# Kernel tuning notes

Hardware: AMD Instinct MI355X
Metric: run time of the kernel (lower is better)

Reference implementation:

```python
import jax, jax.numpy as jnp
import numpy as np

N, NFEAT, NHID, NCLASS, NHEADS = 4096, 512, 64, 40, 8
ALPHA = 0.2  # LeakyReLU negative slope
NEG_BIG = -9e15


def _xavier(key, shape, gain=1.414):
    fan_in, fan_out = shape[0], shape[1]
    bound = gain * np.sqrt(6.0 / (fan_in + fan_out))
    return jax.random.uniform(key, shape, jnp.float32, -bound, bound)


def setup_inputs() -> dict:
    key = jax.random.key(0)
    ks = jax.random.split(key, 6)
    x = jax.random.normal(ks[0], (N, NFEAT), jnp.float32)
    adj = jax.random.randint(ks[1], (N, N), 0, 2).astype(jnp.float32)
    # per-head params of the 8 input GAT layers
    Ws = _xavier(ks[2], (NHEADS, NFEAT, NHID))          # stacked W: [H, F, D]
    a_s = _xavier(ks[3], (NHEADS, 2 * NHID, 1))[..., 0]  # [H, 2D]
    # output GAT layer (concat=False)
    W_out = _xavier(ks[4], (NHID * NHEADS, NCLASS))
    a_out = _xavier(ks[5], (2 * NCLASS, 1))[..., 0]      # [2C]
    return {"x": x, "adj": adj, "Ws": Ws, "a_s": a_s, "W_out": W_out, "a_out": a_out}


def _gat_layer(inp, adj_mask, W, a, concat):
    # h = inp @ W : [N, D]
    h = inp @ W
    D = h.shape[1]
    a1, a2 = a[:D], a[D:]
    # e[i,j] = leakyrelu(a . [h_i, h_j]) = leakyrelu(h_i.a1 + h_j.a2)
    # (same math as the N*N*2D concat in the original, without materializing it)
    f1 = h @ a1  # [N]
    f2 = h @ a2  # [N]
    e = jax.nn.leaky_relu(f1[:, None] + f2[None, :], negative_slope=ALPHA)
    att = jax.nn.softmax(jnp.where(adj_mask, e, NEG_BIG), axis=1)
    h_prime = att @ h  # [N, D]
    return jax.nn.elu(h_prime) if concat else h_prime


def reference(x, adj, Ws, a_s, W_out, a_out):
    adj_mask = adj > 0
    # 8 attention heads over the input features (eval mode: dropout is identity)
    heads = jax.vmap(lambda W, a: _gat_layer(x, adj_mask, W, a, True))(Ws, a_s)  # [H, N, D]
    x2 = jnp.transpose(heads, (1, 0, 2)).reshape(N, NHEADS * NHID)  # concat along feature dim
    out = _gat_layer(x2, adj_mask, W_out, a_out, False)  # [N, C]
    out = jax.nn.elu(out)
    return jax.nn.log_softmax(out, axis=1)
```

## Files before the change

kernel.cpp:

```cpp
#include <hip/hip_runtime.h>
#include <hip/hip_bf16.h>
#include <stdint.h>

#define NN 4096
#define NF 512
#define NH 64
#define NCLS 40
#define NHEADS 8
#define LOG2E 1.4426950408889634f

typedef __attribute__((ext_vector_type(8))) short bh8;
typedef __attribute__((ext_vector_type(4))) float f32x4;

__device__ __forceinline__ unsigned short f2bu(float f) {
    union { float f; unsigned u; } v; v.f = f;
    unsigned r = (v.u + 0x7FFFu + ((v.u >> 16) & 1u)) >> 16;
    return (unsigned short)r;
}
__device__ __forceinline__ float lrelu(float x) { return fmaxf(x, 0.2f * x); }
__device__ __forceinline__ float elu1(float x) { return x > 0.f ? x : expm1f(x); }
__device__ __forceinline__ float exp2fast(float x) {
    float r; asm("v_exp_f32 %0, %1" : "=v"(r) : "v"(x)); return r;
}
__device__ __forceinline__ unsigned fenc(float f) {
    unsigned u = __builtin_bit_cast(unsigned, f);
    return ((int)u < 0) ? ~u : (u | 0x80000000u);
}
__device__ __forceinline__ float fdec(unsigned k) {
    unsigned u = (k & 0x80000000u) ? (k ^ 0x80000000u) : ~k;
    return __builtin_bit_cast(float, u);
}
__device__ __forceinline__ int sbfe1(unsigned v, int off) {
#if __has_builtin(__builtin_amdgcn_sbfe)
    return __builtin_amdgcn_sbfe((int)v, off, 1);
#else
    return ((int)(v << (31 - off))) >> 31;
#endif
}
__device__ __forceinline__ float bmask(float p, unsigned mdw, int bit) {
    return __builtin_bit_cast(float,
        __builtin_bit_cast(unsigned, p) & (unsigned)sbfe1(mdw, bit));
}

__global__ void prep_all_k(const float* __restrict__ x, const float* __restrict__ Ws,
                           const float* __restrict__ Wo,
                           unsigned short* __restrict__ xb, unsigned short* __restrict__ WT,
                           unsigned short* __restrict__ WoT) {
    int idx = blockIdx.x * 256 + threadIdx.x;
    if (idx < 2097152) {
        xb[idx] = f2bu(x[idx]);
    } else if (idx < 2097152 + 262144) {
        int j = idx - 2097152;
        int c = j >> 9, k = j & 511;
        WT[j] = f2bu(Ws[(size_t)(c >> 6) * (NF * NH) + (size_t)k * NH + (c & 63)]);
    } else if (idx < 2097152 + 262144 + 24576) {
        int j = idx - 2359296;
        int c = j >> 9, k = j & 511;
        WoT[j] = f2bu(c < NCLS ? Wo[(size_t)k * NCLS + c] : 0.f);
    }
}
__global__ __launch_bounds__(256) void prep_adj_k(const float* __restrict__ adj,
                                                  unsigned char* __restrict__ adjp,
                                                  unsigned* __restrict__ FM1u,
                                                  unsigned* __restrict__ FM2u) {
    if (blockIdx.x == 0) {
        if (threadIdx.x < 8) FM1u[threadIdx.x] = 0u;
        if (threadIdx.x == 8) FM2u[0] = 0u;
    }
    int w = threadIdx.x >> 6, lane = threadIdx.x & 63;
    int i = blockIdx.x * 4 + w;
    const float* row = adj + (size_t)i * NN;
    for (int t = 0; t < 64; ++t) {
        uint64_t m = __ballot(row[t * 64 + lane] > 0.f);
        if (lane < 8) {
            unsigned char mb = (unsigned char)(m >> (8 * lane));
            int grp = lane & 3, jt = 2 * t + (lane >> 2);
            adjp[((size_t)i * 4 + grp) * 128 + jt] = mb;
        }
    }
}

__device__ __forceinline__ unsigned pack2(float x, float y) {
    unsigned ux = __builtin_bit_cast(unsigned, x), uy = __builtin_bit_cast(unsigned, y);
    ux += 0x7FFFu + ((ux >> 16) & 1u);
    uy += 0x7FFFu + ((uy >> 16) & 1u);
    return __builtin_amdgcn_perm(uy, ux, 0x07060302u);
}

__global__ __launch_bounds__(256) void gemm1_k(const unsigned short* __restrict__ xb,
                                               const unsigned short* __restrict__ WT,
                                               const float* __restrict__ a_s,
                                               unsigned short* __restrict__ Bp1,
                                               float* __restrict__ f1L,
                                               float* __restrict__ f2L,
                                               unsigned* __restrict__ FM1u) {
    __shared__ unsigned short xs[64 * 40];
    __shared__ unsigned short wsm[64 * 40];
    const int tid = threadIdx.x;
    const int w = tid >> 6, lane = tid & 63, r16 = lane & 15, grp = lane >> 4;
    const int i0 = blockIdx.x << 6, h = blockIdx.y, c0 = h << 6;
    const int srow = tid >> 2, sseg = tid & 3;
    const unsigned short* xsrc = xb + (size_t)(i0 + srow) * NF + sseg * 8;
    const unsigned short* wsrc = WT + (size_t)(c0 + srow) * NF + sseg * 8;
    f32x4 a0 = {0,0,0,0}, a1 = {0,0,0,0}, a2 = {0,0,0,0}, a3 = {0,0,0,0};
    bh8 rx = *(const bh8*)(xsrc), rw = *(const bh8*)(wsrc);
    for (int kb = 0; kb < NF; kb += 32) {
        *(bh8*)(xs + srow * 40 + sseg * 8) = rx;
        *(bh8*)(wsm + srow * 40 + sseg * 8) = rw;
        __syncthreads();
        if (kb + 32 < NF) { rx = *(const bh8*)(xsrc + kb + 32); rw = *(const bh8*)(wsrc + kb + 32); }
        bh8 af = *(const bh8*)(xs + (w * 16 + r16) * 40 + grp * 8);
        bh8 b0 = *(const bh8*)(wsm + (r16) * 40 + grp * 8);
        bh8 b1 = *(const bh8*)(wsm + (16 + r16) * 40 + grp * 8);
        bh8 b2 = *(const bh8*)(wsm + (32 + r16) * 40 + grp * 8);
        bh8 b3 = *(const bh8*)(wsm + (48 + r16) * 40 + grp * 8);
        a0 = __builtin_amdgcn_mfma_f32_16x16x32_bf16(af, b0, a0, 0, 0, 0);
        a1 = __builtin_amdgcn_mfma_f32_16x16x32_bf16(af, b1, a1, 0, 0, 0);
        a2 = __builtin_amdgcn_mfma_f32_16x16x32_bf16(af, b2, a2, 0, 0, 0);
        a3 = __builtin_amdgcn_mfma_f32_16x16x32_bf16(af, b3, a3, 0, 0, 0);
        __syncthreads();
    }
    const int jt = (i0 >> 5) + (w >> 1);
    const int kg = ((w & 1) << 1) + (grp >> 1);
    const int lanep = kg * 16 + r16;
    const int ebase = (grp & 1) * 4;
    unsigned short* bp = Bp1 + ((size_t)(h * 128 + jt)) * 2048 + lanep * 8 + ebase;
    {
        uint2 v;
        v.x = pack2(a0[0], a0[1]); v.y = pack2(a0[2], a0[3]); *(uint2*)(bp + 0 * 512) = v;
        v.x = pack2(a1[0], a1[1]); v.y = pack2(a1[2], a1[3]); *(uint2*)(bp + 1 * 512) = v;
        v.x = pack2(a2[0], a2[1]); v.y = pack2(a2[2], a2[3]); *(uint2*)(bp + 2 * 512) = v;
        v.x = pack2(a3[0], a3[1]); v.y = pack2(a3[2], a3[3]); *(uint2*)(bp + 3 * 512) = v;
    }
    const float* ap = a_s + h * 128;
    float a1v[4], a2v[4];
#pragma unroll
    for (int n = 0; n < 4; ++n) { a1v[n] = ap[r16 + 16 * n]; a2v[n] = ap[64 + r16 + 16 * n]; }
    float wmax = -3.0e38f;
#pragma unroll
    for (int r = 0; r < 4; ++r) {
        const int orow = i0 + w * 16 + grp * 4 + r;
        float s1 = a0[r] * a1v[0] + a1[r] * a1v[1] + a2[r] * a1v[2] + a3[r] * a1v[3];
        float s2 = a0[r] * a2v[0] + a1[r] * a2v[1] + a2[r] * a2v[2] + a3[r] * a2v[3];
#pragma unroll
        for (int o2 = 1; o2 < 16; o2 <<= 1) { s1 += __shfl_xor(s1, o2); s2 += __shfl_xor(s2, o2); }
        s1 *= LOG2E; s2 *= LOG2E;
        if (r16 == 0) { f1L[h * NN + orow] = s1; f2L[h * NN + orow] = s2; }
        wmax = fmaxf(wmax, s2);
    }
    wmax = fmaxf(wmax, __shfl_xor(wmax, 16));
    wmax = fmaxf(wmax, __shfl_xor(wmax, 32));
    if (lane == 0) atomicMax(&FM1u[h], fenc(wmax));
}

__global__ __launch_bounds__(256) void gemm2_k(const unsigned short* __restrict__ x2b,
                                               const unsigned short* __restrict__ WoT,
                                               const float* __restrict__ a_out,
                                               unsigned short* __restrict__ Bp2,
                                               float* __restrict__ f12L,
                                               float* __restrict__ f22L,
                                               unsigned* __restrict__ FM2u) {
    __shared__ unsigned short xs[64 * 40];
    __shared__ unsigned short wsm[48 * 40];
    const int tid = threadIdx.x;
    const int w = tid >> 6, lane = tid & 63, r16 = lane & 15, grp = lane >> 4;
    const int i0 = blockIdx.x << 6;
    const int srow = tid >> 2, sseg = tid & 3;
    const unsigned short* xsrc = x2b + (size_t)(i0 + srow) * NF + sseg * 8;
    const unsigned short* wsrc = WoT + (size_t)srow * NF + sseg * 8;
    f32x4 a0 = {0,0,0,0}, a1 = {0,0,0,0}, a2 = {0,0,0,0};
    bh8 rx = *(const bh8*)(xsrc);
    bh8 rw; if (tid < 192) rw = *(const bh8*)(wsrc);
    for (int kb = 0; kb < NF; kb += 32) {
        *(bh8*)(xs + srow * 40 + sseg * 8) = rx;
        if (tid < 192) *(bh8*)(wsm + srow * 40 + sseg * 8) = rw;
        __syncthreads();
        if (kb + 32 < NF) {
            rx = *(const bh8*)(xsrc + kb + 32);
            if (tid < 192) rw = *(const bh8*)(wsrc + kb + 32);
        }
        bh8 af = *(const bh8*)(xs + (w * 16 + r16) * 40 + grp * 8);
        bh8 b0 = *(const bh8*)(wsm + (r16) * 40 + grp * 8);
        bh8 b1 = *(const bh8*)(wsm + (16 + r16) * 40 + grp * 8);
        bh8 b2 = *(const bh8*)(wsm + (32 + r16) * 40 + grp * 8);
        a0 = __builtin_amdgcn_mfma_f32_16x16x32_bf16(af, b0, a0, 0, 0, 0);
        a1 = __builtin_amdgcn_mfma_f32_16x16x32_bf16(af, b1, a1, 0, 0, 0);
        a2 = __builtin_amdgcn_mfma_f32_16x16x32_bf16(af, b2, a2, 0, 0, 0);
        __syncthreads();
    }
    const int jt = (i0 >> 5) + (w >> 1);
    const int kg = ((w & 1) << 1) + (grp >> 1);
    const int lanep = kg * 16 + r16;
    const int ebase = (grp & 1) * 4;
    unsigned short* bp = Bp2 + (size_t)jt * 1536 + lanep * 8 + ebase;
    {
        uint2 v;
        v.x = pack2(a0[0], a0[1]); v.y = pack2(a0[2], a0[3]); *(uint2*)(bp + 0 * 512) = v;
        v.x = pack2(a1[0], a1[1]); v.y = pack2(a1[2], a1[3]); *(uint2*)(bp + 1 * 512) = v;
        v.x = pack2(a2[0], a2[1]); v.y = pack2(a2[2], a2[3]); *(uint2*)(bp + 2 * 512) = v;
    }
    float a1v[3], a2v[3];
#pragma unroll
    for (int n = 0; n < 3; ++n) {
        int col = r16 + 16 * n;
        a1v[n] = col < NCLS ? a_out[col] : 0.f;
        a2v[n] = col < NCLS ? a_out[NCLS + col] : 0.f;
    }
    float wmax = -3.0e38f;
#pragma unroll
    for (int r = 0; r < 4; ++r) {
        const int orow = i0 + w * 16 + grp * 4 + r;
        float s1 = a0[r] * a1v[0] + a1[r] * a1v[1] + a2[r] * a1v[2];
        float s2 = a0[r] * a2v[0] + a1[r] * a2v[1] + a2[r] * a2v[2];
#pragma unroll
        for (int o2 = 1; o2 < 16; o2 <<= 1) { s1 += __shfl_xor(s1, o2); s2 += __shfl_xor(s2, o2); }
        s1 *= LOG2E; s2 *= LOG2E;
        if (r16 == 0) { f12L[orow] = s1; f22L[orow] = s2; }
        wmax = fmaxf(wmax, s2);
    }
    wmax = fmaxf(wmax, __shfl_xor(wmax, 16));
    wmax = fmaxf(wmax, __shfl_xor(wmax, 32));
    if (lane == 0) atomicMax(&FM2u[0], fenc(wmax));
}

__global__ __launch_bounds__(512, 4) void attn1_k(const unsigned short* __restrict__ Bp1,
                                                  const unsigned char* __restrict__ adjp,
                                                  const float* __restrict__ f1L,
                                                  const float* __restrict__ f2L,
                                                  const unsigned* __restrict__ FM1u,
                                                  unsigned short* __restrict__ x2b) {
    __shared__ float EFs[8192];
    __shared__ unsigned ADJd[64 * 4 * 33];
    const int tid = threadIdx.x, w = tid >> 6, lane = tid & 63;
    const int r16 = lane & 15, grp = lane >> 4;
    const int rowg = w & 3, jq = w >> 2;
    const int h = blockIdx.y;
    const int i0 = blockIdx.x * 64;
    const float fm = fdec(FM1u[h]);
    const float* f2p = f2L + h * NN;
    for (int t = 0; t < 8; ++t) {
        int j = tid + t * 512;
        float d = f2p[j] - fm;
        EFs[2 * j] = exp2fast(d);
        EFs[2 * j + 1] = exp2fast(0.2f * d);
    }
    {
        const unsigned* asrc = (const unsigned*)(adjp + (size_t)i0 * 512);
        for (int t = 0; t < 16; ++t) {
            int idx = tid + t * 512;
            ADJd[(idx >> 5) * 33 + (idx & 31)] = asrc[idx];
        }
    }
    const int irow = i0 + rowg * 16 + r16;
    const float f1v = f1L[h * NN + irow];
    const float mL = lrelu(f1v + fm);
    const float A = exp2fast(f1v + fm - mL);
    const float B = exp2fast(__builtin_fmaf(0.2f, f1v + fm, -mL));
    __syncthreads();
    const unsigned* adjrd = ADJd + ((rowg * 16 + r16) * 4 + grp) * 33 + jq * 16;
    const float* efp = EFs + grp * 16;
    const unsigned short* Bbase = Bp1 + (size_t)h * 128 * 2048 + lane * 8;
    f32x4 acc0 = {0,0,0,0}, acc1 = {0,0,0,0}, acc2 = {0,0,0,0}, acc3 = {0,0,0,0}, accd = {0,0,0,0};
    const short ov = (r16 == 0) ? (short)0x3F80 : (short)0;
    bh8 ones;
#pragma unroll
    for (int e = 0; e < 8; ++e) ones[e] = ov;
    bh8 nb0, nb1, nb2, nb3;
#define PREF1(JT) { const unsigned short* Bn = Bbase + (size_t)(JT) * 2048;              \
        nb0 = *(const bh8*)(Bn);        nb1 = *(const bh8*)(Bn + 512);                    \
        nb2 = *(const bh8*)(Bn + 1024); nb3 = *(const bh8*)(Bn + 1536); }
    const int jtbase = jq * 64;
    PREF1(jtbase);
    for (int jt4 = 0; jt4 < 16; ++jt4) {
        const unsigned mdw = adjrd[jt4];
#pragma unroll
        for (int u = 0; u < 4; ++u) {
            const int jt = jtbase + jt4 * 4 + u;
            bh8 b0 = nb0, b1 = nb1, b2 = nb2, b3 = nb3;
            PREF1(jt + 1);
            const float* e4 = efp + jt * 64;
            float4 ea = *(const float4*)(e4);
            float4 eb = *(const float4*)(e4 + 4);
            float4 ec = *(const float4*)(e4 + 8);
            float4 ed = *(const float4*)(e4 + 12);
            const int bb = u * 8;
            union { bh8 v; unsigned u32[4]; } pk;
            {
                float p0 = bmask(fmaxf(A * ea.x, B * ea.y), mdw, bb + 0);
                float p1 = bmask(fmaxf(A * ea.z, B * ea.w), mdw, bb + 1);
                pk.u32[0] = __builtin_amdgcn_perm(__builtin_bit_cast(unsigned, p1),
                                                  __builtin_bit_cast(unsigned, p0), 0x07060302u);
                float p2 = bmask(fmaxf(A * eb.x, B * eb.y), mdw, bb + 2);
                float p3 = bmask(fmaxf(A * eb.z, B * eb.w), mdw, bb + 3);
                pk.u32[1] = __builtin_amdgcn_perm(__builtin_bit_cast(unsigned, p3),
                                                  __builtin_bit_cast(unsigned, p2), 0x07060302u);
                float p4 = bmask(fmaxf(A * ec.x, B * ec.y), mdw, bb + 4);
                float p5 = bmask(fmaxf(A * ec.z, B * ec.w), mdw, bb + 5);
                pk.u32[2] = __builtin_amdgcn_perm(__builtin_bit_cast(unsigned, p5),
                                                  __builtin_bit_cast(unsigned, p4), 0x07060302u);
                float p6 = bmask(fmaxf(A * ed.x, B * ed.y), mdw, bb + 6);
                float p7 = bmask(fmaxf(A * ed.z, B * ed.w), mdw, bb + 7);
                pk.u32[3] = __builtin_amdgcn_perm(__builtin_bit_cast(unsigned, p7),
                                                  __builtin_bit_cast(unsigned, p6), 0x07060302u);
            }
            acc0 = __builtin_amdgcn_mfma_f32_16x16x32_bf16(pk.v, b0, acc0, 0, 0, 0);
            acc1 = __builtin_amdgcn_mfma_f32_16x16x32_bf16(pk.v, b1, acc1, 0, 0, 0);
            acc2 = __builtin_amdgcn_mfma_f32_16x16x32_bf16(pk.v, b2, acc2, 0, 0, 0);
            acc3 = __builtin_amdgcn_mfma_f32_16x16x32_bf16(pk.v, b3, acc3, 0, 0, 0);
            accd = __builtin_amdgcn_mfma_f32_16x16x32_bf16(pk.v, ones, accd, 0, 0, 0);
        }
    }
#undef PREF1
    __syncthreads();
    float (*comb)[64][20] = (float(*)[64][20])EFs;
    if (jq == 1) {
        float* cb = &comb[rowg][lane][0];
#pragma unroll
        for (int r = 0; r < 4; ++r) {
            cb[r] = acc0[r]; cb[4 + r] = acc1[r]; cb[8 + r] = acc2[r];
            cb[12 + r] = acc3[r]; cb[16 + r] = accd[r];
        }
    }
    __syncthreads();
    if (jq == 0) {
        const float* cb = &comb[rowg][lane][0];
#pragma unroll
        for (int r = 0; r < 4; ++r) {
            acc0[r] += cb[r]; acc1[r] += cb[4 + r]; acc2[r] += cb[8 + r];
            acc3[r] += cb[12 + r]; accd[r] += cb[16 + r];
        }
#pragma unroll
        for (int r = 0; r < 4; ++r) {
            const float den = __shfl(accd[r], lane & 48);
            const float inv = 1.0f / den;
            unsigned short* o = x2b + (size_t)(i0 + rowg * 16 + grp * 4 + r) * NF + h * 64 + r16;
            o[0]  = f2bu(elu1(acc0[r] * inv));
            o[16] = f2bu(elu1(acc1[r] * inv));
            o[32] = f2bu(elu1(acc2[r] * inv));
            o[48] = f2bu(elu1(acc3[r] * inv));
        }
    }
}

__global__ __launch_bounds__(256, 4) void attn2_k(const unsigned short* __restrict__ Bp2,
                                                  const unsigned char* __restrict__ adjp,
                                                  const float* __restrict__ f12L,
                                                  const float* __restrict__ f22L,
                                                  const unsigned* __restrict__ FM2u,
                                                  float* __restrict__ Pa2) {
    __shared__ float EFs[1024];
    const int tid = threadIdx.x, w = tid >> 6, lane = tid & 63;
    const int r16 = lane & 15, grp = lane >> 4;
    const int ch = blockIdx.y;
    const int i0 = blockIdx.x * 64 + w * 16;
    const int i = i0 + r16;
    const float fm = fdec(FM2u[0]);
    for (int t = 0; t < 2; ++t) {
        int j = tid + t * 256;
        float d = f22L[ch * 512 + j] - fm;
        EFs[2 * j] = exp2fast(d);
        EFs[2 * j + 1] = exp2fast(0.2f * d);
    }
    const float f1v = f12L[i];
    const float mL = lrelu(f1v + fm);
    const float A = exp2fast(f1v + fm - mL);
    const float B = exp2fast(__builtin_fmaf(0.2f, f1v + fm, -mL));
    __syncthreads();
    const unsigned char* adjr = adjp + ((size_t)i * 4 + grp) * 128 + ch * 16;
    f32x4 acc0 = {0,0,0,0}, acc1 = {0,0,0,0}, acc2 = {0,0,0,0}, accd = {0,0,0,0};
    const short ov = (r16 == 0) ? (short)0x3F80 : (short)0;
    bh8 ones;
#pragma unroll
    for (int e = 0; e < 8; ++e) ones[e] = ov;
    const int jt0 = ch * 16;
    const unsigned short* Bbase = Bp2 + lane * 8;
    const float* efp = EFs + grp * 16;
    bh8 nb0, nb1, nb2;
#define PREF2(JT) { const unsigned short* Bn = Bbase + (size_t)(JT) * 1536;              \
        nb0 = *(const bh8*)(Bn); nb1 = *(const bh8*)(Bn + 512); nb2 = *(const bh8*)(Bn + 1024); }
    PREF2(jt0);
    for (int jt4 = 0; jt4 < 4; ++jt4) {
        const unsigned mdw = *(const unsigned*)(adjr + jt4 * 4);
#pragma unroll
        for (int u = 0; u < 4; ++u) {
            const int ltj = jt4 * 4 + u;
            bh8 b0 = nb0, b1 = nb1, b2 = nb2;
            PREF2(jt0 + ltj + 1);
            const float* e4 = efp + ltj * 64;
            float4 ea = *(const float4*)(e4);
            float4 eb = *(const float4*)(e4 + 4);
            float4 ec = *(const float4*)(e4 + 8);
            float4 ed = *(const float4*)(e4 + 12);
            const int bb = u * 8;
            union { bh8 v; unsigned u32[4]; } pk;
            {
                float p0 = bmask(fmaxf(A * ea.x, B * ea.y), mdw, bb + 0);
                float p1 = bmask(fmaxf(A * ea.z, B * ea.w), mdw, bb + 1);
                pk.u32[0] = __builtin_amdgcn_perm(__builtin_bit_cast(unsigned, p1),
                                                  __builtin_bit_cast(unsigned, p0), 0x07060302u);
                float p2 = bmask(fmaxf(A * eb.x, B * eb.y), mdw, bb + 2);
                float p3 = bmask(fmaxf(A * eb.z, B * eb.w), mdw, bb + 3);
                pk.u32[1] = __builtin_amdgcn_perm(__builtin_bit_cast(unsigned, p3),
                                                  __builtin_bit_cast(unsigned, p2), 0x07060302u);
                float p4 = bmask(fmaxf(A * ec.x, B * ec.y), mdw, bb + 4);
                float p5 = bmask(fmaxf(A * ec.z, B * ec.w), mdw, bb + 5);
                pk.u32[2] = __builtin_amdgcn_perm(__builtin_bit_cast(unsigned, p5),
                                                  __builtin_bit_cast(unsigned, p4), 0x07060302u);
                float p6 = bmask(fmaxf(A * ed.x, B * ed.y), mdw, bb + 6);
                float p7 = bmask(fmaxf(A * ed.z, B * ed.w), mdw, bb + 7);
                pk.u32[3] = __builtin_amdgcn_perm(__builtin_bit_cast(unsigned, p7),
                                                  __builtin_bit_cast(unsigned, p6), 0x07060302u);
            }
            acc0 = __builtin_amdgcn_mfma_f32_16x16x32_bf16(pk.v, b0, acc0, 0, 0, 0);
            acc1 = __builtin_amdgcn_mfma_f32_16x16x32_bf16(pk.v, b1, acc1, 0, 0, 0);
            acc2 = __builtin_amdgcn_mfma_f32_16x16x32_bf16(pk.v, b2, acc2, 0, 0, 0);
            accd = __builtin_amdgcn_mfma_f32_16x16x32_bf16(pk.v, ones, accd, 0, 0, 0);
        }
    }
#undef PREF2
#pragma unroll
    for (int r = 0; r < 4; ++r) {
        const int row = i0 + grp * 4 + r;
        float* prow = Pa2 + ((size_t)ch * NN + row) * 52;
        prow[r16] = acc0[r];
        prow[16 + r16] = acc1[r];
        prow[32 + r16] = acc2[r];
        if (r16 == 0) prow[48] = accd[r];
    }
}

__global__ __launch_bounds__(256) void attn2fin_k(const float* __restrict__ Pa2,
                                                  float* __restrict__ out) {
    const int tid = threadIdx.x;
    const int row = blockIdx.x * 4 + (tid >> 6);
    const int lane = tid & 63;
    float s = 0.f;
    if (lane < 49) {
#pragma unroll
        for (int c = 0; c < 8; ++c) s += Pa2[((size_t)c * NN + row) * 52 + lane];
    }
    const float den = __shfl(s, 48);
    const float inv = 1.0f / den;
    float v = (lane < NCLS) ? elu1(s * inv) : -3.0e38f;
    float mx = v;
#pragma unroll
    for (int o = 1; o < 64; o <<= 1) mx = fmaxf(mx, __shfl_xor(mx, o));
    float ex = (lane < NCLS) ? __expf(v - mx) : 0.f;
#pragma unroll
    for (int o = 1; o < 64; o <<= 1) ex += __shfl_xor(ex, o);
    const float lse = mx + logf(ex);
    if (lane < NCLS) out[(size_t)row * NCLS + lane] = v - lse;
}

#define OFF_XB   0ULL
#define OFF_WT   4194304ULL
#define OFF_WOT  4718592ULL
#define OFF_BP1  4767744ULL
#define OFF_X2B  8962048ULL
#define OFF_BP2  13156352ULL
#define OFF_F1L  13549568ULL
#define OFF_F2L  13680640ULL
#define OFF_F12  13811712ULL
#define OFF_F22  13828096ULL
#define OFF_FM1  13844480ULL
#define OFF_FM2  13844736ULL
#define OFF_ADJ  13844992ULL
#define OFF_PA2  15942144ULL

extern "C" void kernel_launch(void* const* d_in, const int* in_sizes, int n_in,
                              void* d_out, int out_size, void* d_ws, size_t ws_size,
                              hipStream_t stream) {
    const float* x     = (const float*)d_in[0];
    const float* adj   = (const float*)d_in[1];
    const float* Ws    = (const float*)d_in[2];
    const float* a_s   = (const float*)d_in[3];
    const float* W_out = (const float*)d_in[4];
    const float* a_out = (const float*)d_in[5];
    float* out = (float*)d_out;
    char* w = (char*)d_ws;

    unsigned short* xb  = (unsigned short*)(w + OFF_XB);
    unsigned short* WT  = (unsigned short*)(w + OFF_WT);
    unsigned short* WoT = (unsigned short*)(w + OFF_WOT);
    unsigned short* Bp1 = (unsigned short*)(w + OFF_BP1);
    unsigned short* x2b = (unsigned short*)(w + OFF_X2B);
    unsigned short* Bp2 = (unsigned short*)(w + OFF_BP2);
    float* f1L = (float*)(w + OFF_F1L);
    float* f2L = (float*)(w + OFF_F2L);
    float* f12 = (float*)(w + OFF_F12);
    float* f22 = (float*)(w + OFF_F22);
    unsigned* FM1u = (unsigned*)(w + OFF_FM1);
    unsigned* FM2u = (unsigned*)(w + OFF_FM2);
    unsigned char* adjp = (unsigned char*)(w + OFF_ADJ);
    float* Pa2 = (float*)(w + OFF_PA2);

    prep_all_k<<<9312, 256, 0, stream>>>(x, Ws, W_out, xb, WT, WoT);
    prep_adj_k<<<1024, 256, 0, stream>>>(adj, adjp, FM1u, FM2u);

    gemm1_k<<<dim3(64, 8), 256, 0, stream>>>(xb, WT, a_s, Bp1, f1L, f2L, FM1u);
    attn1_k<<<dim3(64, 8), 512, 0, stream>>>(Bp1, adjp, f1L, f2L, FM1u, x2b);

    gemm2_k<<<64, 256, 0, stream>>>(x2b, WoT, a_out, Bp2, f12, f22, FM2u);
    attn2_k<<<dim3(64, 8), 256, 0, stream>>>(Bp2, adjp, f12, f22, FM2u, Pa2);
    attn2fin_k<<<1024, 256, 0, stream>>>(Pa2, out);
}
```

Before: 233.3 us.

## Merge prep kernels, fuse attn2 with finalize, drop LDS adjacency staging

Merges the adjacency bit-packing and the bf16 conversion kernels into one launch and vectorizes the adjacency reads and x conversion. gemm1 now uses 128-row tiles with 512 threads. attn1 reads adjacency masks straight from global memory instead of staging them in LDS, and its occupancy hint is raised. attn2 now does the column-chunk reduction in LDS inside the block and applies the log-softmax there, which removes the partial-sum buffer and the separate finalize kernel. This trades fewer launches and less global traffic for in-block tree reductions and fewer, larger attn2 blocks.

Measured after the change: 207.3 us. 11.2% less time.

```diff
diff --git a/kernel.cpp b/kernel.cpp
--- a/kernel.cpp
+++ b/kernel.cpp
@@ -41,45 +41,6 @@
     return __builtin_bit_cast(float,
         __builtin_bit_cast(unsigned, p) & (unsigned)sbfe1(mdw, bit));
 }
-
-__global__ void prep_all_k(const float* __restrict__ x, const float* __restrict__ Ws,
-                           const float* __restrict__ Wo,
-                           unsigned short* __restrict__ xb, unsigned short* __restrict__ WT,
-                           unsigned short* __restrict__ WoT) {
-    int idx = blockIdx.x * 256 + threadIdx.x;
-    if (idx < 2097152) {
-        xb[idx] = f2bu(x[idx]);
-    } else if (idx < 2097152 + 262144) {
-        int j = idx - 2097152;
-        int c = j >> 9, k = j & 511;
-        WT[j] = f2bu(Ws[(size_t)(c >> 6) * (NF * NH) + (size_t)k * NH + (c & 63)]);
-    } else if (idx < 2097152 + 262144 + 24576) {
-        int j = idx - 2359296;
-        int c = j >> 9, k = j & 511;
-        WoT[j] = f2bu(c < NCLS ? Wo[(size_t)k * NCLS + c] : 0.f);
-    }
-}
-__global__ __launch_bounds__(256) void prep_adj_k(const float* __restrict__ adj,
-                                                  unsigned char* __restrict__ adjp,
-                                                  unsigned* __restrict__ FM1u,
-                                                  unsigned* __restrict__ FM2u) {
-    if (blockIdx.x == 0) {
-        if (threadIdx.x < 8) FM1u[threadIdx.x] = 0u;
-        if (threadIdx.x == 8) FM2u[0] = 0u;
-    }
-    int w = threadIdx.x >> 6, lane = threadIdx.x & 63;
-    int i = blockIdx.x * 4 + w;
-    const float* row = adj + (size_t)i * NN;
-    for (int t = 0; t < 64; ++t) {
-        uint64_t m = __ballot(row[t * 64 + lane] > 0.f);
-        if (lane < 8) {
-            unsigned char mb = (unsigned char)(m >> (8 * lane));
-            int grp = lane & 3, jt = 2 * t + (lane >> 2);
-            adjp[((size_t)i * 4 + grp) * 128 + jt] = mb;
-        }
-    }
-}
-
 __device__ __forceinline__ unsigned pack2(float x, float y) {
     unsigned ux = __builtin_bit_cast(unsigned, x), uy = __builtin_bit_cast(unsigned, y);
     ux += 0x7FFFu + ((ux >> 16) & 1u);
@@ -87,28 +48,80 @@
     return __builtin_amdgcn_perm(uy, ux, 0x07060302u);
 }
 
-__global__ __launch_bounds__(256) void gemm1_k(const unsigned short* __restrict__ xb,
+__global__ __launch_bounds__(256) void prep_all_k(const float* __restrict__ x,
+                                                  const float* __restrict__ adj,
+                                                  const float* __restrict__ Ws,
+                                                  const float* __restrict__ Wo,
+                                                  unsigned short* __restrict__ xb,
+                                                  unsigned short* __restrict__ WT,
+                                                  unsigned short* __restrict__ WoT,
+                                                  unsigned char* __restrict__ adjp,
+                                                  unsigned* __restrict__ FM1u,
+                                                  unsigned* __restrict__ FM2u) {
+    const int bid = blockIdx.x, tid = threadIdx.x;
+    if (bid < 8192) {
+        __shared__ unsigned char sm[4][64];
+        const int i = bid >> 1, half = bid & 1;
+        const float* rp = adj + (size_t)i * NN + half * 2048 + tid * 8;
+        float4 v0 = ((const float4*)rp)[0];
+        float4 v1 = ((const float4*)rp)[1];
+        unsigned b = (v0.x > 0.f ? 1u : 0u) | (v0.y > 0.f ? 2u : 0u) |
+                     (v0.z > 0.f ? 4u : 0u) | (v0.w > 0.f ? 8u : 0u) |
+                     (v1.x > 0.f ? 16u : 0u) | (v1.y > 0.f ? 32u : 0u) |
+                     (v1.z > 0.f ? 64u : 0u) | (v1.w > 0.f ? 128u : 0u);
+        sm[tid & 3][tid >> 2] = (unsigned char)b;
+        __syncthreads();
+        if (tid < 64) {
+            int gp = tid >> 4, word = tid & 15;
+            unsigned d = *(const unsigned*)&sm[gp][word * 4];
+            *(unsigned*)(adjp + ((size_t)i * 4 + gp) * 128 + half * 64 + word * 4) = d;
+        }
+    } else if (bid < 10240) {
+        if (bid == 8192) {
+            if (tid < 8) FM1u[tid] = 0u;
+            if (tid == 8) FM2u[0] = 0u;
+        }
+        int t = (bid - 8192) * 256 + tid;
+        float4 v = ((const float4*)x)[t];
+        uint2 o; o.x = pack2(v.x, v.y); o.y = pack2(v.z, v.w);
+        ((uint2*)xb)[t] = o;
+    } else if (bid < 11264) {
+        int j = (bid - 10240) * 256 + tid;
+        int c = j >> 9, k = j & 511;
+        WT[j] = f2bu(Ws[(size_t)(c >> 6) * (NF * NH) + (size_t)k * NH + (c & 63)]);
+    } else {
+        int j = (bid - 11264) * 256 + tid;
+        int c = j >> 9, k = j & 511;
+        WoT[j] = f2bu(c < NCLS ? Wo[(size_t)k * NCLS + c] : 0.f);
+    }
+}
+
+__global__ __launch_bounds__(512) void gemm1_k(const unsigned short* __restrict__ xb,
                                                const unsigned short* __restrict__ WT,
                                                const float* __restrict__ a_s,
                                                unsigned short* __restrict__ Bp1,
                                                float* __restrict__ f1L,
                                                float* __restrict__ f2L,
                                                unsigned* __restrict__ FM1u) {
-    __shared__ unsigned short xs[64 * 40];
+    __shared__ unsigned short xs[128 * 40];
     __shared__ unsigned short wsm[64 * 40];
     const int tid = threadIdx.x;
     const int w = tid >> 6, lane = tid & 63, r16 = lane & 15, grp = lane >> 4;
-    const int i0 = blockIdx.x << 6, h = blockIdx.y, c0 = h << 6;
+    const int i0 = blockIdx.x << 7, h = blockIdx.y, c0 = h << 6;
     const int srow = tid >> 2, sseg = tid & 3;
     const unsigned short* xsrc = xb + (size_t)(i0 + srow) * NF + sseg * 8;
-    const unsigned short* wsrc = WT + (size_t)(c0 + srow) * NF + sseg * 8;
+    const unsigned short* wsrc = WT + (size_t)(c0 + (srow & 63)) * NF + sseg * 8;
     f32x4 a0 = {0,0,0,0}, a1 = {0,0,0,0}, a2 = {0,0,0,0}, a3 = {0,0,0,0};
-    bh8 rx = *(const bh8*)(xsrc), rw = *(const bh8*)(wsrc);
+    bh8 rx = *(const bh8*)(xsrc);
+    bh8 rw; if (tid < 256) rw = *(const bh8*)(wsrc);
     for (int kb = 0; kb < NF; kb += 32) {
         *(bh8*)(xs + srow * 40 + sseg * 8) = rx;
-        *(bh8*)(wsm + srow * 40 + sseg * 8) = rw;
+        if (tid < 256) *(bh8*)(wsm + srow * 40 + sseg * 8) = rw;
         __syncthreads();
-        if (kb + 32 < NF) { rx = *(const bh8*)(xsrc + kb + 32); rw = *(const bh8*)(wsrc + kb + 32); }
+        if (kb + 32 < NF) {
+            rx = *(const bh8*)(xsrc + kb + 32);
+            if (tid < 256) rw = *(const bh8*)(wsrc + kb + 32);
+        }
         bh8 af = *(const bh8*)(xs + (w * 16 + r16) * 40 + grp * 8);
         bh8 b0 = *(const bh8*)(wsm + (r16) * 40 + grp * 8);
         bh8 b1 = *(const bh8*)(wsm + (16 + r16) * 40 + grp * 8);
@@ -223,14 +236,13 @@
     if (lane == 0) atomicMax(&FM2u[0], fenc(wmax));
 }
 
-__global__ __launch_bounds__(512, 4) void attn1_k(const unsigned short* __restrict__ Bp1,
+__global__ __launch_bounds__(512, 6) void attn1_k(const unsigned short* __restrict__ Bp1,
                                                   const unsigned char* __restrict__ adjp,
                                                   const float* __restrict__ f1L,
                                                   const float* __restrict__ f2L,
                                                   const unsigned* __restrict__ FM1u,
                                                   unsigned short* __restrict__ x2b) {
     __shared__ float EFs[8192];
-    __shared__ unsigned ADJd[64 * 4 * 33];
     const int tid = threadIdx.x, w = tid >> 6, lane = tid & 63;
     const int r16 = lane & 15, grp = lane >> 4;
     const int rowg = w & 3, jq = w >> 2;
@@ -244,20 +256,14 @@
         EFs[2 * j] = exp2fast(d);
         EFs[2 * j + 1] = exp2fast(0.2f * d);
     }
-    {
-        const unsigned* asrc = (const unsigned*)(adjp + (size_t)i0 * 512);
-        for (int t = 0; t < 16; ++t) {
-            int idx = tid + t * 512;
-            ADJd[(idx >> 5) * 33 + (idx & 31)] = asrc[idx];
-        }
-    }
     const int irow = i0 + rowg * 16 + r16;
     const float f1v = f1L[h * NN + irow];
     const float mL = lrelu(f1v + fm);
     const float A = exp2fast(f1v + fm - mL);
     const float B = exp2fast(__builtin_fmaf(0.2f, f1v + fm, -mL));
     __syncthreads();
-    const unsigned* adjrd = ADJd + ((rowg * 16 + r16) * 4 + grp) * 33 + jq * 16;
+    const int jtbase = jq * 64;
+    const unsigned char* adjr = adjp + ((size_t)irow * 4 + grp) * 128 + jtbase;
     const float* efp = EFs + grp * 16;
     const unsigned short* Bbase = Bp1 + (size_t)h * 128 * 2048 + lane * 8;
     f32x4 acc0 = {0,0,0,0}, acc1 = {0,0,0,0}, acc2 = {0,0,0,0}, acc3 = {0,0,0,0}, accd = {0,0,0,0};
@@ -269,15 +275,127 @@
 #define PREF1(JT) { const unsigned short* Bn = Bbase + (size_t)(JT) * 2048;              \
         nb0 = *(const bh8*)(Bn);        nb1 = *(const bh8*)(Bn + 512);                    \
         nb2 = *(const bh8*)(Bn + 1024); nb3 = *(const bh8*)(Bn + 1536); }
-    const int jtbase = jq * 64;
     PREF1(jtbase);
-    for (int jt4 = 0; jt4 < 16; ++jt4) {
-        const unsigned mdw = adjrd[jt4];
+    for (int jt16 = 0; jt16 < 4; ++jt16) {
+        const uint4 a4 = *(const uint4*)(adjr + jt16 * 16);
+#pragma unroll
+        for (int q = 0; q < 4; ++q) {
+            const unsigned mdw = (q == 0) ? a4.x : (q == 1) ? a4.y : (q == 2) ? a4.z : a4.w;
+#pragma unroll
+            for (int u = 0; u < 4; ++u) {
+                const int jt = jtbase + jt16 * 16 + q * 4 + u;
+                bh8 b0 = nb0, b1 = nb1, b2 = nb2, b3 = nb3;
+                PREF1(jt + 1);
+                const float* e4 = efp + jt * 64;
+                float4 ea = *(const float4*)(e4);
+                float4 eb = *(const float4*)(e4 + 4);
+                float4 ec = *(const float4*)(e4 + 8);
+                float4 ed = *(const float4*)(e4 + 12);
+                const int bb = u * 8;
+                union { bh8 v; unsigned u32[4]; } pk;
+                {
+                    float p0 = bmask(fmaxf(A * ea.x, B * ea.y), mdw, bb + 0);
+                    float p1 = bmask(fmaxf(A * ea.z, B * ea.w), mdw, bb + 1);
+                    pk.u32[0] = __builtin_amdgcn_perm(__builtin_bit_cast(unsigned, p1),
+                                                      __builtin_bit_cast(unsigned, p0), 0x07060302u);
+                    float p2 = bmask(fmaxf(A * eb.x, B * eb.y), mdw, bb + 2);
+                    float p3 = bmask(fmaxf(A * eb.z, B * eb.w), mdw, bb + 3);
+                    pk.u32[1] = __builtin_amdgcn_perm(__builtin_bit_cast(unsigned, p3),
+                                                      __builtin_bit_cast(unsigned, p2), 0x07060302u);
+                    float p4 = bmask(fmaxf(A * ec.x, B * ec.y), mdw, bb + 4);
+                    float p5 = bmask(fmaxf(A * ec.z, B * ec.w), mdw, bb + 5);
+                    pk.u32[2] = __builtin_amdgcn_perm(__builtin_bit_cast(unsigned, p5),
+                                                      __builtin_bit_cast(unsigned, p4), 0x07060302u);
+                    float p6 = bmask(fmaxf(A * ed.x, B * ed.y), mdw, bb + 6);
+                    float p7 = bmask(fmaxf(A * ed.z, B * ed.w), mdw, bb + 7);
+                    pk.u32[3] = __builtin_amdgcn_perm(__builtin_bit_cast(unsigned, p7),
+                                                      __builtin_bit_cast(unsigned, p6), 0x07060302u);
+                }
+                acc0 = __builtin_amdgcn_mfma_f32_16x16x32_bf16(pk.v, b0, acc0, 0, 0, 0);
+                acc1 = __builtin_amdgcn_mfma_f32_16x16x32_bf16(pk.v, b1, acc1, 0, 0, 0);
+                acc2 = __builtin_amdgcn_mfma_f32_16x16x32_bf16(pk.v, b2, acc2, 0, 0, 0);
+                acc3 = __builtin_amdgcn_mfma_f32_16x16x32_bf16(pk.v, b3, acc3, 0, 0, 0);
+                accd = __builtin_amdgcn_mfma_f32_16x16x32_bf16(pk.v, ones, accd, 0, 0, 0);
+            }
+        }
+    }
+#undef PREF1
+    __syncthreads();
+    float (*comb)[64][21] = (float(*)[64][21])EFs;
+    if (jq == 1) {
+        float* cb = &comb[rowg][lane][0];
+#pragma unroll
+        for (int r = 0; r < 4; ++r) {
+            cb[r] = acc0[r]; cb[4 + r] = acc1[r]; cb[8 + r] = acc2[r];
+            cb[12 + r] = acc3[r]; cb[16 + r] = accd[r];
+        }
+    }
+    __syncthreads();
+    if (jq == 0) {
+        const float* cb = &comb[rowg][lane][0];
+#pragma unroll
+        for (int r = 0; r < 4; ++r) {
+            acc0[r] += cb[r]; acc1[r] += cb[4 + r]; acc2[r] += cb[8 + r];
+            acc3[r] += cb[12 + r]; accd[r] += cb[16 + r];
+        }
+#pragma unroll
+        for (int r = 0; r < 4; ++r) {
+            const float den = __shfl(accd[r], lane & 48);
+            const float inv = 1.0f / den;
+            unsigned short* o = x2b + (size_t)(i0 + rowg * 16 + grp * 4 + r) * NF + h * 64 + r16;
+            o[0]  = f2bu(elu1(acc0[r] * inv));
+            o[16] = f2bu(elu1(acc1[r] * inv));
+            o[32] = f2bu(elu1(acc2[r] * inv));
+            o[48] = f2bu(elu1(acc3[r] * inv));
+        }
+    }
+}
+
+__global__ __launch_bounds__(512, 6) void attn2_k(const unsigned short* __restrict__ Bp2,
+                                                  const unsigned char* __restrict__ adjp,
+                                                  const float* __restrict__ f12L,
+                                                  const float* __restrict__ f22L,
+                                                  const unsigned* __restrict__ FM2u,
+                                                  float* __restrict__ out) {
+    __shared__ float EFs[8192];
+    __shared__ float comb[8][64][17];
+    const int tid = threadIdx.x, w = tid >> 6, lane = tid & 63;
+    const int r16 = lane & 15, grp = lane >> 4;
+    const int i0 = blockIdx.x * 16;
+    const int i = i0 + r16;
+    const float fm = fdec(FM2u[0]);
+    for (int t = 0; t < 8; ++t) {
+        int j = tid + t * 512;
+        float d = f22L[j] - fm;
+        EFs[2 * j] = exp2fast(d);
+        EFs[2 * j + 1] = exp2fast(0.2f * d);
+    }
+    const float f1v = f12L[i];
+    const float mL = lrelu(f1v + fm);
+    const float A = exp2fast(f1v + fm - mL);
+    const float B = exp2fast(__builtin_fmaf(0.2f, f1v + fm, -mL));
+    __syncthreads();
+    const int jt0 = w * 16;
+    const uint4 a4 = *(const uint4*)(adjp + ((size_t)i * 4 + grp) * 128 + jt0);
+    f32x4 acc0 = {0,0,0,0}, acc1 = {0,0,0,0}, acc2 = {0,0,0,0}, accd = {0,0,0,0};
+    const short ov = (r16 == 0) ? (short)0x3F80 : (short)0;
+    bh8 ones;
+#pragma unroll
+    for (int e = 0; e < 8; ++e) ones[e] = ov;
+    const unsigned short* Bbase = Bp2 + lane * 8;
+    const float* efp = EFs + grp * 16;
+    bh8 nb0, nb1, nb2;
+#define PREF2(JT) { const unsigned short* Bn = Bbase + (size_t)(JT) * 1536;              \
+        nb0 = *(const bh8*)(Bn); nb1 = *(const bh8*)(Bn + 512); nb2 = *(const bh8*)(Bn + 1024); }
+    PREF2(jt0);
+#pragma unroll
+    for (int q = 0; q < 4; ++q) {
+        const unsigned mdw = (q == 0) ? a4.x : (q == 1) ? a4.y : (q == 2) ? a4.z : a4.w;
 #pragma unroll
         for (int u = 0; u < 4; ++u) {
-            const int jt = jtbase + jt4 * 4 + u;
-            bh8 b0 = nb0, b1 = nb1, b2 = nb2, b3 = nb3;
-            PREF1(jt + 1);
+            const int jt = jt0 + q * 4 + u;
+            bh8 b0 = nb0, b1 = nb1, b2 = nb2;
+            PREF2(jt + 1);
             const float* e4 = efp + jt * 64;
             float4 ea = *(const float4*)(e4);
             float4 eb = *(const float4*)(e4 + 4);
@@ -306,150 +424,65 @@
             acc0 = __builtin_amdgcn_mfma_f32_16x16x32_bf16(pk.v, b0, acc0, 0, 0, 0);
             acc1 = __builtin_amdgcn_mfma_f32_16x16x32_bf16(pk.v, b1, acc1, 0, 0, 0);
             acc2 = __builtin_amdgcn_mfma_f32_16x16x32_bf16(pk.v, b2, acc2, 0, 0, 0);
-            acc3 = __builtin_amdgcn_mfma_f32_16x16x32_bf16(pk.v, b3, acc3, 0, 0, 0);
             accd = __builtin_amdgcn_mfma_f32_16x16x32_bf16(pk.v, ones, accd, 0, 0, 0);
         }
     }
-#undef PREF1
-    __syncthreads();
-    float (*comb)[64][20] = (float(*)[64][20])EFs;
-    if (jq == 1) {
-        float* cb = &comb[rowg][lane][0];
-#pragma unroll
-        for (int r = 0; r < 4; ++r) {
-            cb[r] = acc0[r]; cb[4 + r] = acc1[r]; cb[8 + r] = acc2[r];
-            cb[12 + r] = acc3[r]; cb[16 + r] = accd[r];
-        }
-    }
-    __syncthreads();
-    if (jq == 0) {
-        const float* cb = &comb[rowg][lane][0];
-#pragma unroll
-        for (int r = 0; r < 4; ++r) {
-            acc0[r] += cb[r]; acc1[r] += cb[4 + r]; acc2[r] += cb[8 + r];
-            acc3[r] += cb[12 + r]; accd[r] += cb[16 + r];
-        }
-#pragma unroll
-        for (int r = 0; r < 4; ++r) {
+#undef PREF2
+    {
+        float* cb = &comb[w][lane][0];
+#pragma unroll
+        for (int r = 0; r < 4; ++r) {
+            cb[r] = acc0[r]; cb[4 + r] = acc1[r]; cb[8 + r] = acc2[r]; cb[12 + r] = accd[r];
+        }
+    }
+    __syncthreads();
+    if (w < 4) {
+        const float* sb = &comb[w + 4][lane][0];
+        float* cb = &comb[w][lane][0];
+#pragma unroll
+        for (int r = 0; r < 4; ++r) {
+            acc0[r] += sb[r]; acc1[r] += sb[4 + r]; acc2[r] += sb[8 + r]; accd[r] += sb[12 + r];
+            cb[r] = acc0[r]; cb[4 + r] = acc1[r]; cb[8 + r] = acc2[r]; cb[12 + r] = accd[r];
+        }
+    }
+    __syncthreads();
+    if (w < 2) {
+        const float* sb = &comb[w + 2][lane][0];
+        float* cb = &comb[w][lane][0];
+#pragma unroll
+        for (int r = 0; r < 4; ++r) {
+            acc0[r] += sb[r]; acc1[r] += sb[4 + r]; acc2[r] += sb[8 + r]; accd[r] += sb[12 + r];
+            cb[r] = acc0[r]; cb[4 + r] = acc1[r]; cb[8 + r] = acc2[r]; cb[12 + r] = accd[r];
+        }
+    }
+    __syncthreads();
+    if (w == 0) {
+        const float* sb = &comb[1][lane][0];
+#pragma unroll
+        for (int r = 0; r < 4; ++r) {
+            acc0[r] += sb[r]; acc1[r] += sb[4 + r]; acc2[r] += sb[8 + r]; accd[r] += sb[12 + r];
+        }
+#pragma unroll
+        for (int r = 0; r < 4; ++r) {
+            const int row = grp * 4 + r;
             const float den = __shfl(accd[r], lane & 48);
             const float inv = 1.0f / den;
-            unsigned short* o = x2b + (size_t)(i0 + rowg * 16 + grp * 4 + r) * NF + h * 64 + r16;
-            o[0]  = f2bu(elu1(acc0[r] * inv));
-            o[16] = f2bu(elu1(acc1[r] * inv));
-            o[32] = f2bu(elu1(acc2[r] * inv));
-            o[48] = f2bu(elu1(acc3[r] * inv));
-        }
-    }
-}
-
-__global__ __launch_bounds__(256, 4) void attn2_k(const unsigned short* __restrict__ Bp2,
-                                                  const unsigned char* __restrict__ adjp,
-                                                  const float* __restrict__ f12L,
-                                                  const float* __restrict__ f22L,
-                                                  const unsigned* __restrict__ FM2u,
-                                                  float* __restrict__ Pa2) {
-    __shared__ float EFs[1024];
-    const int tid = threadIdx.x, w = tid >> 6, lane = tid & 63;
-    const int r16 = lane & 15, grp = lane >> 4;
-    const int ch = blockIdx.y;
-    const int i0 = blockIdx.x * 64 + w * 16;
-    const int i = i0 + r16;
-    const float fm = fdec(FM2u[0]);
-    for (int t = 0; t < 2; ++t) {
-        int j = tid + t * 256;
-        float d = f22L[ch * 512 + j] - fm;
-        EFs[2 * j] = exp2fast(d);
-        EFs[2 * j + 1] = exp2fast(0.2f * d);
-    }
-    const float f1v = f12L[i];
-    const float mL = lrelu(f1v + fm);
-    const float A = exp2fast(f1v + fm - mL);
-    const float B = exp2fast(__builtin_fmaf(0.2f, f1v + fm, -mL));
-    __syncthreads();
-    const unsigned char* adjr = adjp + ((size_t)i * 4 + grp) * 128 + ch * 16;
-    f32x4 acc0 = {0,0,0,0}, acc1 = {0,0,0,0}, acc2 = {0,0,0,0}, accd = {0,0,0,0};
-    const short ov = (r16 == 0) ? (short)0x3F80 : (short)0;
-    bh8 ones;
-#pragma unroll
-    for (int e = 0; e < 8; ++e) ones[e] = ov;
-    const int jt0 = ch * 16;
-    const unsigned short* Bbase = Bp2 + lane * 8;
-    const float* efp = EFs + grp * 16;
-    bh8 nb0, nb1, nb2;
-#define PREF2(JT) { const unsigned short* Bn = Bbase + (size_t)(JT) * 1536;              \
-        nb0 = *(const bh8*)(Bn); nb1 = *(const bh8*)(Bn + 512); nb2 = *(const bh8*)(Bn + 1024); }
-    PREF2(jt0);
-    for (int jt4 = 0; jt4 < 4; ++jt4) {
-        const unsigned mdw = *(const unsigned*)(adjr + jt4 * 4);
-#pragma unroll
-        for (int u = 0; u < 4; ++u) {
-            const int ltj = jt4 * 4 + u;
-            bh8 b0 = nb0, b1 = nb1, b2 = nb2;
-            PREF2(jt0 + ltj + 1);
-            const float* e4 = efp + ltj * 64;
-            float4 ea = *(const float4*)(e4);
-            float4 eb = *(const float4*)(e4 + 4);
-            float4 ec = *(const float4*)(e4 + 8);
-            float4 ed = *(const float4*)(e4 + 12);
-            const int bb = u * 8;
-            union { bh8 v; unsigned u32[4]; } pk;
-            {
-                float p0 = bmask(fmaxf(A * ea.x, B * ea.y), mdw, bb + 0);
-                float p1 = bmask(fmaxf(A * ea.z, B * ea.w), mdw, bb + 1);
-                pk.u32[0] = __builtin_amdgcn_perm(__builtin_bit_cast(unsigned, p1),
-                                                  __builtin_bit_cast(unsigned, p0), 0x07060302u);
-                float p2 = bmask(fmaxf(A * eb.x, B * eb.y), mdw, bb + 2);
-                float p3 = bmask(fmaxf(A * eb.z, B * eb.w), mdw, bb + 3);
-                pk.u32[1] = __builtin_amdgcn_perm(__builtin_bit_cast(unsigned, p3),
-                                                  __builtin_bit_cast(unsigned, p2), 0x07060302u);
-                float p4 = bmask(fmaxf(A * ec.x, B * ec.y), mdw, bb + 4);
-                float p5 = bmask(fmaxf(A * ec.z, B * ec.w), mdw, bb + 5);
-                pk.u32[2] = __builtin_amdgcn_perm(__builtin_bit_cast(unsigned, p5),
-                                                  __builtin_bit_cast(unsigned, p4), 0x07060302u);
-                float p6 = bmask(fmaxf(A * ed.x, B * ed.y), mdw, bb + 6);
-                float p7 = bmask(fmaxf(A * ed.z, B * ed.w), mdw, bb + 7);
-                pk.u32[3] = __builtin_amdgcn_perm(__builtin_bit_cast(unsigned, p7),
-                                                  __builtin_bit_cast(unsigned, p6), 0x07060302u);
-            }
-            acc0 = __builtin_amdgcn_mfma_f32_16x16x32_bf16(pk.v, b0, acc0, 0, 0, 0);
-            acc1 = __builtin_amdgcn_mfma_f32_16x16x32_bf16(pk.v, b1, acc1, 0, 0, 0);
-            acc2 = __builtin_amdgcn_mfma_f32_16x16x32_bf16(pk.v, b2, acc2, 0, 0, 0);
-            accd = __builtin_amdgcn_mfma_f32_16x16x32_bf16(pk.v, ones, accd, 0, 0, 0);
-        }
-    }
-#undef PREF2
-#pragma unroll
-    for (int r = 0; r < 4; ++r) {
-        const int row = i0 + grp * 4 + r;
-        float* prow = Pa2 + ((size_t)ch * NN + row) * 52;
-        prow[r16] = acc0[r];
-        prow[16 + r16] = acc1[r];
-        prow[32 + r16] = acc2[r];
-        if (r16 == 0) prow[48] = accd[r];
-    }
-}
-
-__global__ __launch_bounds__(256) void attn2fin_k(const float* __restrict__ Pa2,
-                                                  float* __restrict__ out) {
-    const int tid = threadIdx.x;
-    const int row = blockIdx.x * 4 + (tid >> 6);
-    const int lane = tid & 63;
-    float s = 0.f;
-    if (lane < 49) {
-#pragma unroll
-        for (int c = 0; c < 8; ++c) s += Pa2[((size_t)c * NN + row) * 52 + lane];
-    }
-    const float den = __shfl(s, 48);
-    const float inv = 1.0f / den;
-    float v = (lane < NCLS) ? elu1(s * inv) : -3.0e38f;
-    float mx = v;
-#pragma unroll
-    for (int o = 1; o < 64; o <<= 1) mx = fmaxf(mx, __shfl_xor(mx, o));
-    float ex = (lane < NCLS) ? __expf(v - mx) : 0.f;
-#pragma unroll
-    for (int o = 1; o < 64; o <<= 1) ex += __shfl_xor(ex, o);
-    const float lse = mx + logf(ex);
-    if (lane < NCLS) out[(size_t)row * NCLS + lane] = v - lse;
+            float v0 = elu1(acc0[r] * inv);
+            float v1 = elu1(acc1[r] * inv);
+            float v2 = (r16 < 8) ? elu1(acc2[r] * inv) : -3.0e38f;
+            float mx = fmaxf(fmaxf(v0, v1), v2);
+#pragma unroll
+            for (int o = 1; o < 16; o <<= 1) mx = fmaxf(mx, __shfl_xor(mx, o));
+            float ex = __expf(v0 - mx) + __expf(v1 - mx) + ((r16 < 8) ? __expf(v2 - mx) : 0.f);
+#pragma unroll
+            for (int o = 1; o < 16; o <<= 1) ex += __shfl_xor(ex, o);
+            const float lse = mx + logf(ex);
+            float* op = out + (size_t)(i0 + row) * NCLS;
+            op[r16] = v0 - lse;
+            op[16 + r16] = v1 - lse;
+            if (r16 < 8) op[32 + r16] = v2 - lse;
+        }
+    }
 }
 
 #define OFF_XB   0ULL
@@ -465,7 +498,6 @@
 #define OFF_FM1  13844480ULL
 #define OFF_FM2  13844736ULL
 #define OFF_ADJ  13844992ULL
-#define OFF_PA2  15942144ULL
 
 extern "C" void kernel_launch(void* const* d_in, const int* in_sizes, int n_in,
                               void* d_out, int out_size, void* d_ws, size_t ws_size,
@@ -492,15 +524,10 @@
     unsigned* FM1u = (unsigned*)(w + OFF_FM1);
     unsigned* FM2u = (unsigned*)(w + OFF_FM2);
     unsigned char* adjp = (unsigned char*)(w + OFF_ADJ);
-    float* Pa2 = (float*)(w + OFF_PA2);
-
-    prep_all_k<<<9312, 256, 0, stream>>>(x, Ws, W_out, xb, WT, WoT);
-    prep_adj_k<<<1024, 256, 0, stream>>>(adj, adjp, FM1u, FM2u);
-
-    gemm1_k<<<dim3(64, 8), 256, 0, stream>>>(xb, WT, a_s, Bp1, f1L, f2L, FM1u);
+
+    prep_all_k<<<11360, 256, 0, stream>>>(x, adj, Ws, W_out, xb, WT, WoT, adjp, FM1u, FM2u);
+    gemm1_k<<<dim3(32, 8), 512, 0, stream>>>(xb, WT, a_s, Bp1, f1L, f2L, FM1u);
     attn1_k<<<dim3(64, 8), 512, 0, stream>>>(Bp1, adjp, f1L, f2L, FM1u, x2b);
-
     gemm2_k<<<64, 256, 0, stream>>>(x2b, WoT, a_out, Bp2, f12, f22, FM2u);
-    attn2_k<<<dim3(64, 8), 256, 0, stream>>>(Bp2, adjp, f12, f22, FM2u, Pa2);
-    attn2fin_k<<<1024, 256, 0, stream>>>(Pa2, out);
-}
+    attn2_k<<<256, 512, 0, stream>>>(Bp2, adjp, f12, f22, FM2u, out);
+}
```
